# Optimization experiments

Hardware: AMD Instinct MI355X
Metric: run time of the kernel (lower is better)

The kernel has to match this reference:

```python
import jax, jax.numpy as jnp
import numpy as np

HEAD_SIZE = 20
NUM_HEADS = 2


def setup_inputs() -> dict:
    key = jax.random.key(0)
    k1, k2, k3, k4, k5, k6 = jax.random.split(key, 6)
    N, L, D = 32, 256, HEAD_SIZE
    x = jax.random.normal(k1, (N, N, L, D), dtype=jnp.float32)
    y = jax.random.normal(k2, (N, N, L, D), dtype=jnp.float32)
    s = 1.0 / np.sqrt(D)
    WQ = jax.random.normal(k3, (D, HEAD_SIZE * NUM_HEADS), dtype=jnp.float32) * s
    WK = jax.random.normal(k4, (D, HEAD_SIZE * NUM_HEADS), dtype=jnp.float32) * s
    WV = jax.random.normal(k5, (D, HEAD_SIZE * NUM_HEADS), dtype=jnp.float32) * s
    WH = jax.random.normal(k6, (HEAD_SIZE * NUM_HEADS, HEAD_SIZE), dtype=jnp.float32) * s
    return {"x": x, "y": y, "WQ": WQ, "WK": WK, "WV": WV, "WH": WH}


def _masked_softmax(logits):
    # mask wherever the raw logit is exactly zero (custom zero-value mask)
    mask = logits != 0
    z = jnp.exp(logits - jnp.max(logits, axis=-1, keepdims=True))
    z = jnp.where(mask, z, jnp.zeros_like(z))
    return z / (jnp.sum(z, axis=-1, keepdims=True) + 1e-10)


def reference(x, y, WQ, WK, WV, WH):
    nSet_x, nSet_y, Lx, D = x.shape
    Ly = y.shape[2]
    H, Dh = NUM_HEADS, HEAD_SIZE
    scale = 1.0 / jnp.sqrt(jnp.asarray(Dh, dtype=jnp.float32))

    # cross branch: transpose x [1,0,2,3] then flatten set dims
    xq = jnp.transpose(x, (1, 0, 2, 3)).reshape(-1, Lx, D)  # [B, Lx, D]
    yf = y.reshape(-1, Ly, D)                               # [B, Ly, D]

    q = xq @ WQ   # [B, Lx, H*Dh]
    k = yf @ WK   # [B, Ly, H*Dh]
    v = yf @ WV   # [B, Ly, H*Dh]

    B = q.shape[0]
    q = q.reshape(B, Lx, H, Dh).transpose(0, 2, 1, 3)  # [B, H, Lx, Dh]
    k = k.reshape(B, Ly, H, Dh).transpose(0, 2, 1, 3)
    v = v.reshape(B, Ly, H, Dh).transpose(0, 2, 1, 3)

    logits = jnp.einsum('bhqd,bhkd->bhqk', q, k) * scale  # [B, H, Lx, Ly]
    attn = _masked_softmax(logits)
    o = jnp.einsum('bhqk,bhkd->bhqd', attn, v)            # [B, H, Lx, Dh]
    o = o.transpose(0, 2, 1, 3).reshape(B, Lx, H * Dh)
    out = o @ WH                                          # [B, Lx, Dh]

    out = out.reshape(nSet_x, nSet_y, Lx, Dh).transpose(1, 0, 2, 3)
    return out
```

## Files before the change

### kernel.cpp

```cpp
#include <hip/hip_runtime.h>
#include <stdint.h>


#define NSET 32
#define SEQL 256
#define DM   20
#define NH   2
#define DH   20

typedef __attribute__((ext_vector_type(8))) short short8;
typedef __attribute__((ext_vector_type(4))) short short4v;
typedef __attribute__((ext_vector_type(4))) float f32x4;

#define MFMA32(a, b, c) __builtin_amdgcn_mfma_f32_16x16x32_bf16((a), (b), (c), 0, 0, 0)

#if __has_builtin(__builtin_amdgcn_mfma_f32_16x16x16bf16_1k)
#define MFMA16(a, b, c) __builtin_amdgcn_mfma_f32_16x16x16bf16_1k((a), (b), (c), 0, 0, 0)
#elif __has_builtin(__builtin_amdgcn_mfma_f32_16x16x16_bf16)
#define MFMA16(a, b, c) __builtin_amdgcn_mfma_f32_16x16x16_bf16((a), (b), (c), 0, 0, 0)
#else
static __device__ __forceinline__ f32x4 MFMA16(short4v a, short4v b, f32x4 c) {
    asm volatile("s_nop 1\n\tv_mfma_f32_16x16x16_bf16 %0, %1, %2, %0\n\ts_nop 7"
                 : "+v"(c) : "v"(a), "v"(b));
    return c;
}
#endif

__device__ __forceinline__ uint32_t bfhu(float f) {
    return (__float_as_uint(f) + 0x8000u) >> 16;
}
__device__ __forceinline__ uint32_t packbf(float hi, float lo) {
    return __builtin_amdgcn_perm(__float_as_uint(hi) + 0x8000u,
                                 __float_as_uint(lo) + 0x8000u, 0x07060302u);
}
__device__ __forceinline__ float fexp2(float x) {
    float r;
    asm("v_exp_f32 %0, %1" : "=v"(r) : "v"(x));
    return r;
}

__device__ __forceinline__ short8 ldsA20(const short* base, int row, int qd) {
    uint2 lo = make_uint2(0u, 0u), hi = make_uint2(0u, 0u);
    const short* p = base + row * 20 + qd * 8;
    if (qd < 2) { lo = *(const uint2*)p; hi = *(const uint2*)(p + 4); }
    else if (qd == 2) { lo = *(const uint2*)p; }
    short8 f;
    *(uint2*)&f = lo;
    *(((uint2*)&f) + 1) = hi;
    return f;
}

__device__ __forceinline__ int vtoff(int d, int s) {
    return d * 256 + (s ^ ((d & 7) << 2));
}

__device__ __forceinline__ short8 gfrag(const float* rowp, int qd) {
    short8 f = {0, 0, 0, 0, 0, 0, 0, 0};
    if (qd < 2) {
        float4 a = *(const float4*)(rowp + qd * 8);
        float4 b = *(const float4*)(rowp + qd * 8 + 4);
        f[0] = (short)bfhu(a.x); f[1] = (short)bfhu(a.y);
        f[2] = (short)bfhu(a.z); f[3] = (short)bfhu(a.w);
        f[4] = (short)bfhu(b.x); f[5] = (short)bfhu(b.y);
        f[6] = (short)bfhu(b.z); f[7] = (short)bfhu(b.w);
    } else if (qd == 2) {
        float4 a = *(const float4*)(rowp + 16);
        f[0] = (short)bfhu(a.x); f[1] = (short)bfhu(a.y);
        f[2] = (short)bfhu(a.z); f[3] = (short)bfhu(a.w);
    }
    return f;
}

#define SMEM_BYTES 40960

__global__ __launch_bounds__(512, 4) void set_attn_v12(
    const float* __restrict__ x, const float* __restrict__ y,
    const float* __restrict__ wq, const float* __restrict__ wk,
    const float* __restrict__ wv, const float* __restrict__ wh,
    float* __restrict__ out)
{
    __shared__ __align__(16) char smem[SMEM_BYTES];
    short* sKb  = (short*)smem;
    short* sVtb = (short*)(smem + 20480);
    float* sOut = (float*)smem;

    const int tid     = threadIdx.x;
    const int lane    = tid & 63;
    const int w       = tid >> 6;
    const int c       = lane & 15;
    const int qd      = lane >> 4;
    const int head    = w >> 2;
    const int rowbase = (w & 3) * 64;
    const int b       = blockIdx.x;
    const int bi      = b >> 5, bj = b & 31;

    short* sK  = sKb + head * (SEQL * 20);
    short* sVt = sVtb + head * (20 * 256);
    short* myO = sKb + w * (64 * 20);

    const float QS = 0.22360679774997896f * 1.4426950408889634f;

    short8 xf[4];
#pragma unroll
    for (int mt = 0; mt < 4; ++mt)
        xf[mt] = gfrag(x + ((size_t)b * SEQL + rowbase + mt * 16 + c) * DM, qd);

    short8 wqA0 = {0,0,0,0,0,0,0,0}, wqA1 = wqA0;
#pragma unroll
    for (int j = 0; j < 8; ++j) {
        int k = qd * 8 + j;
        if (k < 20) {
            wqA0[j] = (short)bfhu(wq[k * 40 + head * 20 + c]);
            if (c < 4) wqA1[j] = (short)bfhu(wq[k * 40 + head * 20 + 16 + c]);
        }
    }

    short8 wkf[2], wvf[2];
#pragma unroll
    for (int dt = 0; dt < 2; ++dt) {
        int n = dt * 16 + c;
        short8 fk = {0,0,0,0,0,0,0,0}, fv = fk;
        if (n < 20) {
#pragma unroll
            for (int j = 0; j < 8; ++j) {
                int k = qd * 8 + j;
                if (k < 20) {
                    fk[j] = (short)bfhu(wk[k * 40 + head * 20 + n]);
                    fv[j] = (short)bfhu(wv[k * 40 + head * 20 + n]);
                }
            }
        }
        wkf[dt] = fk; wvf[dt] = fv;
    }

    const int i01 = (c + ((qd & 1) << 5)) << 2;
    const int i23 = (c + 16 + ((qd & 1) << 5)) << 2;
    const int iB  = c << 2;

    short8 qb[4];
#pragma unroll
    for (int mt = 0; mt < 4; ++mt) {
        int rb = rowbase + mt * 16;
        short8 yf = gfrag(y + ((size_t)(bj * NSET + bi) * SEQL + rb + c) * DM, qd);
#pragma unroll
        for (int dt = 0; dt < 2; ++dt) {
            f32x4 z = {0.f, 0.f, 0.f, 0.f};
            f32x4 kres = MFMA32(yf, wkf[dt], z);
            f32x4 vres = MFMA32(yf, wvf[dt], z);
            int n = dt * 16 + c;
            if (n < 20) {
#pragma unroll
                for (int reg = 0; reg < 4; ++reg)
                    sK[(rb + qd * 4 + reg) * 20 + n] = (short)bfhu(kres[reg]);
                uint2 pv = make_uint2(packbf(vres[1], vres[0]),
                                      packbf(vres[3], vres[2]));
                *(uint2*)(sVt + vtoff(n, rb + qd * 4)) = pv;
            }
        }
        {
            f32x4 z = {0.f, 0.f, 0.f, 0.f};
            f32x4 ra = MFMA32(wqA0, xf[mt], z);
            f32x4 rb2 = MFMA32(wqA1, xf[mt], z);
            uint32_t dwA0 = packbf(ra[1] * QS, ra[0] * QS);
            uint32_t dwA1 = packbf(ra[3] * QS, ra[2] * QS);
            uint32_t dwB0 = packbf(rb2[1] * QS, rb2[0] * QS);
            uint32_t dwB1 = packbf(rb2[3] * QS, rb2[2] * QS);
            uint32_t t0a = (uint32_t)__builtin_amdgcn_ds_bpermute(i01, (int)dwA0);
            uint32_t t1a = (uint32_t)__builtin_amdgcn_ds_bpermute(i01, (int)dwA1);
            uint32_t t0b = (uint32_t)__builtin_amdgcn_ds_bpermute(iB, (int)dwB0);
            uint32_t t1b = (uint32_t)__builtin_amdgcn_ds_bpermute(iB, (int)dwB1);
            uint32_t t2  = (uint32_t)__builtin_amdgcn_ds_bpermute(i23, (int)dwA0);
            uint32_t t3  = (uint32_t)__builtin_amdgcn_ds_bpermute(i23, (int)dwA1);
            uint32_t q0 = qd < 2 ? t0a : (qd == 2 ? t0b : 0u);
            uint32_t q1 = qd < 2 ? t1a : (qd == 2 ? t1b : 0u);
            uint32_t q2 = qd < 2 ? t2 : 0u;
            uint32_t q3 = qd < 2 ? t3 : 0u;
            short8 f;
            *(uint2*)&f = make_uint2(q0, q1);
            *(((uint2*)&f) + 1) = make_uint2(q2, q3);
            qb[mt] = f;
        }
    }
    __syncthreads();

    f32x4 oacc[4][2];
#pragma unroll
    for (int mt = 0; mt < 4; ++mt)
#pragma unroll
        for (int dt = 0; dt < 2; ++dt) oacc[mt][dt] = (f32x4){0.f, 0.f, 0.f, 0.f};
    float ls0 = 0.f, ls1 = 0.f, ls2 = 0.f, ls3 = 0.f;

    for (int s0 = 0; s0 < SEQL; s0 += 32) {
        short8 kf0 = ldsA20(sK, s0 + c, qd);
        short8 kf1 = ldsA20(sK, s0 + 16 + c, qd);
        short4v vb[2][2];
#pragma unroll
        for (int dt = 0; dt < 2; ++dt) {
            int d = dt * 16 + c;
#pragma unroll
            for (int st = 0; st < 2; ++st) {
                uint2 u = make_uint2(0u, 0u);
                if (d < 20)
                    u = *(const uint2*)(sVt + vtoff(d, s0 + st * 16 + qd * 4));
                short4v t; *(uint2*)&t = u;
                vb[st][dt] = t;
            }
        }
#pragma unroll
        for (int mt = 0; mt < 4; ++mt) {
#pragma unroll
            for (int st = 0; st < 2; ++st) {
                f32x4 z = {0.f, 0.f, 0.f, 0.f};
                f32x4 sacc = MFMA32((st == 0 ? kf0 : kf1), qb[mt], z);
                float p0, p1, p2, p3;
                {
                    float v0 = sacc[0], v1 = sacc[1], v2 = sacc[2], v3 = sacc[3];
                    p0 = (v0 != 0.f) ? fexp2(v0) : 0.f;
                    p1 = (v1 != 0.f) ? fexp2(v1) : 0.f;
                    p2 = (v2 != 0.f) ? fexp2(v2) : 0.f;
                    p3 = (v3 != 0.f) ? fexp2(v3) : 0.f;
                }
                float lsum = (p0 + p1) + (p2 + p3);
                if (mt == 0) ls0 += lsum;
                else if (mt == 1) ls1 += lsum;
                else if (mt == 2) ls2 += lsum;
                else ls3 += lsum;
                short4v pf;
                *(uint2*)&pf = make_uint2(packbf(p1, p0), packbf(p3, p2));
                oacc[mt][0] = MFMA16(pf, vb[st][0], oacc[mt][0]);
                oacc[mt][1] = MFMA16(pf, vb[st][1], oacc[mt][1]);
            }
        }
    }

    ls0 += __shfl_xor(ls0, 16, 64); ls0 += __shfl_xor(ls0, 32, 64);
    ls1 += __shfl_xor(ls1, 16, 64); ls1 += __shfl_xor(ls1, 32, 64);
    ls2 += __shfl_xor(ls2, 16, 64); ls2 += __shfl_xor(ls2, 32, 64);
    ls3 += __shfl_xor(ls3, 16, 64); ls3 += __shfl_xor(ls3, 32, 64);
    __syncthreads();

    short8 whf[2];
#pragma unroll
    for (int dt = 0; dt < 2; ++dt) {
        int n = dt * 16 + c;
        short8 f = {0,0,0,0,0,0,0,0};
        if (n < 20) {
#pragma unroll
            for (int j = 0; j < 8; ++j) {
                int k = qd * 8 + j;
                if (k < 20) f[j] = (short)bfhu(wh[(head * 20 + k) * 20 + n]);
            }
        }
        whf[dt] = f;
    }
#pragma unroll
    for (int mt = 0; mt < 4; ++mt) {
        float lsm = (mt == 0) ? ls0 : (mt == 1) ? ls1 : (mt == 2) ? ls2 : ls3;
        float inv[4];
#pragma unroll
        for (int reg = 0; reg < 4; ++reg)
            inv[reg] = 1.f / (__shfl(lsm, qd * 4 + reg, 64) + 1e-10f);
#pragma unroll
        for (int dt = 0; dt < 2; ++dt) {
            int n = dt * 16 + c;
            if (n < 20) {
#pragma unroll
                for (int reg = 0; reg < 4; ++reg)
                    myO[(mt * 16 + qd * 4 + reg) * 20 + n] =
                        (short)bfhu(oacc[mt][dt][reg] * inv[reg]);
            }
        }
    }
    __syncthreads();

    f32x4 outacc[4][2];
#pragma unroll
    for (int mt = 0; mt < 4; ++mt) {
        short8 of = ldsA20(myO, mt * 16 + c, qd);
        f32x4 z = {0.f, 0.f, 0.f, 0.f};
        outacc[mt][0] = MFMA32(of, whf[0], z);
        outacc[mt][1] = MFMA32(of, whf[1], z);
    }
    __syncthreads();

    if (head == 1) {
#pragma unroll
        for (int mt = 0; mt < 4; ++mt)
#pragma unroll
            for (int dt = 0; dt < 2; ++dt) {
                int n = dt * 16 + c;
                if (n < 20) {
#pragma unroll
                    for (int reg = 0; reg < 4; ++reg) {
                        int row = rowbase + mt * 16 + qd * 4 + reg;
                        sOut[row * 20 + n] = outacc[mt][dt][reg];
                    }
                }
            }
    }
    __syncthreads();

    if (head == 0) {
        float* ob = out + (size_t)b * (SEQL * DH);
#pragma unroll
        for (int mt = 0; mt < 4; ++mt)
#pragma unroll
            for (int dt = 0; dt < 2; ++dt) {
                int n = dt * 16 + c;
                if (n < 20) {
#pragma unroll
                    for (int reg = 0; reg < 4; ++reg) {
                        int row = rowbase + mt * 16 + qd * 4 + reg;
                        ob[row * 20 + n] = outacc[mt][dt][reg] + sOut[row * 20 + n];
                    }
                }
            }
    }
}

extern "C" void kernel_launch(void* const* d_in, const int* in_sizes, int n_in,
                              void* d_out, int out_size, void* d_ws, size_t ws_size,
                              hipStream_t stream) {
    const float* x  = (const float*)d_in[0];
    const float* y  = (const float*)d_in[1];
    const float* wq = (const float*)d_in[2];
    const float* wk = (const float*)d_in[3];
    const float* wv = (const float*)d_in[4];
    const float* wh = (const float*)d_in[5];
    float* out = (float*)d_out;

    set_attn_v12<<<dim3(NSET * NSET), dim3(512), 0, stream>>>(x, y, wq, wk, wv, wh, out);
}
```

Measured before the change: 146.9 us.

## Fold softmax row sum into PV MFMA via ones column; pack weight gathers

Appends a constant-one row (bf16 1.0) as V^T column 20, so the second PV MFMA tile, whose columns 16-31 were mostly padding, also accumulates the softmax denominator. This removes the per-tile scalar lsum adds and the shuffle reductions; the denominator is read from the accumulator with one shuffle per row. Weight and input fragment gathers now use packed bf16 conversions through helper functions. Shared memory grows slightly, and the sum now comes from bf16-rounded probabilities, which changes numerics a little.

```diff
diff --git a/kernel.cpp b/kernel.cpp
--- a/kernel.cpp
+++ b/kernel.cpp
@@ -59,21 +59,52 @@
     if (qd < 2) {
         float4 a = *(const float4*)(rowp + qd * 8);
         float4 b = *(const float4*)(rowp + qd * 8 + 4);
-        f[0] = (short)bfhu(a.x); f[1] = (short)bfhu(a.y);
-        f[2] = (short)bfhu(a.z); f[3] = (short)bfhu(a.w);
-        f[4] = (short)bfhu(b.x); f[5] = (short)bfhu(b.y);
-        f[6] = (short)bfhu(b.z); f[7] = (short)bfhu(b.w);
+        *(uint2*)&f = make_uint2(packbf(a.y, a.x), packbf(a.w, a.z));
+        *(((uint2*)&f) + 1) = make_uint2(packbf(b.y, b.x), packbf(b.w, b.z));
     } else if (qd == 2) {
         float4 a = *(const float4*)(rowp + 16);
-        f[0] = (short)bfhu(a.x); f[1] = (short)bfhu(a.y);
-        f[2] = (short)bfhu(a.z); f[3] = (short)bfhu(a.w);
+        *(uint2*)&f = make_uint2(packbf(a.y, a.x), packbf(a.w, a.z));
     }
     return f;
 }
 
-#define SMEM_BYTES 40960
-
-__global__ __launch_bounds__(512, 4) void set_attn_v12(
+__device__ __forceinline__ short8 gatherW40(const float* colp, int qd, bool act) {
+    uint32_t u0 = 0u, u1 = 0u, u2 = 0u, u3 = 0u;
+    if (act && qd < 3) {
+        const float* p = colp + qd * 8 * 40;
+        u0 = packbf(p[40], p[0]);
+        u1 = packbf(p[120], p[80]);
+        if (qd < 2) {
+            u2 = packbf(p[200], p[160]);
+            u3 = packbf(p[280], p[240]);
+        }
+    }
+    short8 f;
+    *(uint2*)&f = make_uint2(u0, u1);
+    *(((uint2*)&f) + 1) = make_uint2(u2, u3);
+    return f;
+}
+
+__device__ __forceinline__ short8 gatherW20(const float* colp, int qd, bool act) {
+    uint32_t u0 = 0u, u1 = 0u, u2 = 0u, u3 = 0u;
+    if (act && qd < 3) {
+        const float* p = colp + qd * 8 * 20;
+        u0 = packbf(p[20], p[0]);
+        u1 = packbf(p[60], p[40]);
+        if (qd < 2) {
+            u2 = packbf(p[100], p[80]);
+            u3 = packbf(p[140], p[120]);
+        }
+    }
+    short8 f;
+    *(uint2*)&f = make_uint2(u0, u1);
+    *(((uint2*)&f) + 1) = make_uint2(u2, u3);
+    return f;
+}
+
+#define SMEM_BYTES 41984
+
+__global__ __launch_bounds__(512, 4) void set_attn_v13(
     const float* __restrict__ x, const float* __restrict__ y,
     const float* __restrict__ wq, const float* __restrict__ wk,
     const float* __restrict__ wv, const float* __restrict__ wh,
@@ -95,8 +126,10 @@
     const int bi      = b >> 5, bj = b & 31;
 
     short* sK  = sKb + head * (SEQL * 20);
-    short* sVt = sVtb + head * (20 * 256);
+    short* sVt = sVtb + head * (21 * 256);
     short* myO = sKb + w * (64 * 20);
+
+    sVt[vtoff(20, rowbase + lane)] = (short)0x3F80;
 
     const float QS = 0.22360679774997896f * 1.4426950408889634f;
 
@@ -105,32 +138,15 @@
     for (int mt = 0; mt < 4; ++mt)
         xf[mt] = gfrag(x + ((size_t)b * SEQL + rowbase + mt * 16 + c) * DM, qd);
 
-    short8 wqA0 = {0,0,0,0,0,0,0,0}, wqA1 = wqA0;
-#pragma unroll
-    for (int j = 0; j < 8; ++j) {
-        int k = qd * 8 + j;
-        if (k < 20) {
-            wqA0[j] = (short)bfhu(wq[k * 40 + head * 20 + c]);
-            if (c < 4) wqA1[j] = (short)bfhu(wq[k * 40 + head * 20 + 16 + c]);
-        }
-    }
+    short8 wqA0 = gatherW40(wq + head * 20 + c, qd, true);
+    short8 wqA1 = gatherW40(wq + head * 20 + 16 + c, qd, c < 4);
 
     short8 wkf[2], wvf[2];
 #pragma unroll
     for (int dt = 0; dt < 2; ++dt) {
         int n = dt * 16 + c;
-        short8 fk = {0,0,0,0,0,0,0,0}, fv = fk;
-        if (n < 20) {
-#pragma unroll
-            for (int j = 0; j < 8; ++j) {
-                int k = qd * 8 + j;
-                if (k < 20) {
-                    fk[j] = (short)bfhu(wk[k * 40 + head * 20 + n]);
-                    fv[j] = (short)bfhu(wv[k * 40 + head * 20 + n]);
-                }
-            }
-        }
-        wkf[dt] = fk; wvf[dt] = fv;
+        wkf[dt] = gatherW40(wk + head * 20 + n, qd, n < 20);
+        wvf[dt] = gatherW40(wv + head * 20 + n, qd, n < 20);
     }
 
     const int i01 = (c + ((qd & 1) << 5)) << 2;
@@ -188,7 +204,6 @@
     for (int mt = 0; mt < 4; ++mt)
 #pragma unroll
         for (int dt = 0; dt < 2; ++dt) oacc[mt][dt] = (f32x4){0.f, 0.f, 0.f, 0.f};
-    float ls0 = 0.f, ls1 = 0.f, ls2 = 0.f, ls3 = 0.f;
 
     for (int s0 = 0; s0 < SEQL; s0 += 32) {
         short8 kf0 = ldsA20(sK, s0 + c, qd);
@@ -200,7 +215,7 @@
 #pragma unroll
             for (int st = 0; st < 2; ++st) {
                 uint2 u = make_uint2(0u, 0u);
-                if (d < 20)
+                if (d < 21)
                     u = *(const uint2*)(sVt + vtoff(d, s0 + st * 16 + qd * 4));
                 short4v t; *(uint2*)&t = u;
                 vb[st][dt] = t;
@@ -220,11 +235,6 @@
                     p2 = (v2 != 0.f) ? fexp2(v2) : 0.f;
                     p3 = (v3 != 0.f) ? fexp2(v3) : 0.f;
                 }
-                float lsum = (p0 + p1) + (p2 + p3);
-                if (mt == 0) ls0 += lsum;
-                else if (mt == 1) ls1 += lsum;
-                else if (mt == 2) ls2 += lsum;
-                else ls3 += lsum;
                 short4v pf;
                 *(uint2*)&pf = make_uint2(packbf(p1, p0), packbf(p3, p2));
                 oacc[mt][0] = MFMA16(pf, vb[st][0], oacc[mt][0]);
@@ -232,34 +242,21 @@
             }
         }
     }
-
-    ls0 += __shfl_xor(ls0, 16, 64); ls0 += __shfl_xor(ls0, 32, 64);
-    ls1 += __shfl_xor(ls1, 16, 64); ls1 += __shfl_xor(ls1, 32, 64);
-    ls2 += __shfl_xor(ls2, 16, 64); ls2 += __shfl_xor(ls2, 32, 64);
-    ls3 += __shfl_xor(ls3, 16, 64); ls3 += __shfl_xor(ls3, 32, 64);
     __syncthreads();
 
     short8 whf[2];
 #pragma unroll
     for (int dt = 0; dt < 2; ++dt) {
         int n = dt * 16 + c;
-        short8 f = {0,0,0,0,0,0,0,0};
-        if (n < 20) {
-#pragma unroll
-            for (int j = 0; j < 8; ++j) {
-                int k = qd * 8 + j;
-                if (k < 20) f[j] = (short)bfhu(wh[(head * 20 + k) * 20 + n]);
-            }
-        }
-        whf[dt] = f;
-    }
+        whf[dt] = gatherW20(wh + head * 20 * 20 + n, qd, n < 20);
+    }
+    const int dsrc = (lane & 48) + 4;
 #pragma unroll
     for (int mt = 0; mt < 4; ++mt) {
-        float lsm = (mt == 0) ? ls0 : (mt == 1) ? ls1 : (mt == 2) ? ls2 : ls3;
         float inv[4];
 #pragma unroll
         for (int reg = 0; reg < 4; ++reg)
-            inv[reg] = 1.f / (__shfl(lsm, qd * 4 + reg, 64) + 1e-10f);
+            inv[reg] = 1.f / (__shfl(oacc[mt][1][reg], dsrc, 64) + 1e-10f);
 #pragma unroll
         for (int dt = 0; dt < 2; ++dt) {
             int n = dt * 16 + c;
@@ -329,5 +326,5 @@
     const float* wh = (const float*)d_in[5];
     float* out = (float*)d_out;
 
-    set_attn_v12<<<dim3(NSET * NSET), dim3(512), 0, stream>>>(x, y, wq, wk, wv, wh, out);
-}
+    set_attn_v13<<<dim3(NSET * NSET), dim3(512), 0, stream>>>(x, y, wq, wk, wv, wh, out);
+}
```

Result: faster. 137.7 us (-6.2%).
